# Kernel tuning notes

Hardware: AMD Instinct MI355X
Metric: run time of the kernel (lower is better)

## Reference

```python
import jax, jax.numpy as jnp
import numpy as np

D_MODEL = 1024
D_COND = 512
N_HEADS = 16
D_HEAD = D_MODEL // N_HEADS
DIM_FF = 4 * D_MODEL
EPS = 1e-5


def setup_inputs() -> dict:
    key = jax.random.key(0)
    ks = jax.random.split(key, 12)
    B, S = 2, 2048
    s = 0.02
    return {
        "x": jax.random.normal(ks[0], (B, S, D_MODEL), jnp.float32),
        "cond": jax.random.normal(ks[1], (B, S, D_COND), jnp.float32),
        # AdaLN1 proj (stored as (in, out) so y = h @ W + b)
        "p1_w": jax.random.normal(ks[2], (D_COND, 2 * D_MODEL), jnp.float32) * s,
        "p1_b": jax.random.normal(ks[3], (2 * D_MODEL,), jnp.float32) * s,
        "qkv_w": jax.random.normal(ks[4], (D_MODEL, 3 * D_MODEL), jnp.float32) * s,
        "attn_out_w": jax.random.normal(ks[5], (D_MODEL, D_MODEL), jnp.float32) * s,
        "p2_w": jax.random.normal(ks[6], (D_COND, 2 * D_MODEL), jnp.float32) * s,
        "p2_b": jax.random.normal(ks[7], (2 * D_MODEL,), jnp.float32) * s,
        "ffn_w1": jax.random.normal(ks[8], (D_MODEL, DIM_FF), jnp.float32) * s,
        "ffn_b1": jax.random.normal(ks[9], (DIM_FF,), jnp.float32) * s,
        "ffn_w2": jax.random.normal(ks[10], (DIM_FF, D_MODEL), jnp.float32) * s,
        "ffn_b2": jax.random.normal(ks[11], (D_MODEL,), jnp.float32) * s,
    }


def _adaln(x, cond, w, b):
    # LayerNorm without affine, then (1+gamma)*xn + beta with gamma,beta from cond
    gb = jax.nn.silu(cond) @ w + b            # (B,S,2D)
    gamma, beta = jnp.split(gb, 2, axis=-1)
    mu = jnp.mean(x, axis=-1, keepdims=True)
    var = jnp.mean((x - mu) ** 2, axis=-1, keepdims=True)
    xn = (x - mu) * jax.lax.rsqrt(var + EPS)
    return xn * (1.0 + gamma) + beta


def reference(x, cond, p1_w, p1_b, qkv_w, attn_out_w, p2_w, p2_b,
              ffn_w1, ffn_b1, ffn_w2, ffn_b2):
    B, S, D = x.shape
    H, d = N_HEADS, D_HEAD
    scale = d ** -0.5

    residual = x
    h = _adaln(x, cond, p1_w, p1_b)
    qkv = h @ qkv_w                            # (B,S,3D)
    q, k, v = jnp.split(qkv, 3, axis=-1)
    q = q.reshape(B, S, H, d).transpose(0, 2, 1, 3)   # (B,H,S,d)
    k = k.reshape(B, S, H, d).transpose(0, 2, 1, 3)
    v = v.reshape(B, S, H, d).transpose(0, 2, 1, 3)

    scores = jnp.einsum("bhqd,bhkd->bhqk", q, k) * scale
    attn = jax.nn.softmax(scores, axis=-1)
    out = jnp.einsum("bhqk,bhkd->bhqd", attn, v)      # (B,H,S,d)
    out = out.transpose(0, 2, 1, 3).reshape(B, S, D)
    x = residual + out @ attn_out_w

    residual = x
    h = _adaln(x, cond, p2_w, p2_b)
    ff = jax.nn.gelu(h @ ffn_w1 + ffn_b1, approximate=False) @ ffn_w2 + ffn_b2
    return residual + ff
```

## Files before the change

kernel.cpp:

```cpp
#include <hip/hip_runtime.h>
#include <math.h>

#define D_MODEL 1024
#define SEQ 2048
#define NTOK 4096

typedef __attribute__((ext_vector_type(8))) short bf16x8;
typedef __attribute__((ext_vector_type(4))) float f32x4;

__device__ __forceinline__ unsigned short f2bf(float f) {
    union { float f; unsigned u; } v; v.f = f;
    unsigned r = v.u + 0x7FFFu + ((v.u >> 16) & 1u);
    return (unsigned short)(r >> 16);
}
__device__ __forceinline__ float bf2f(unsigned short u) {
    union { unsigned u; float f; } v; v.u = ((unsigned)u) << 16; return v.f;
}
__device__ __forceinline__ unsigned pk2bf(float x, float y) {
    union { float f; unsigned u; } a, b;
    a.f = x; b.f = y;
    return ((b.u + 0x8000u) & 0xFFFF0000u) | ((a.u + 0x8000u) >> 16);
}

__device__ __forceinline__ void ld_g2l(const void* g, void* l) {
    __builtin_amdgcn_global_load_lds(
        (const __attribute__((address_space(1))) void*)g,
        (__attribute__((address_space(3))) void*)l, 16, 0, 0);
}

__global__ __launch_bounds__(256) void prep_weights(
    const float* __restrict__ p1, const float* __restrict__ p2,
    const float* __restrict__ qkvw, const float* __restrict__ attnw,
    const float* __restrict__ f1, const float* __restrict__ f2,
    const float* __restrict__ cond,
    unsigned short* __restrict__ wt_cond, unsigned short* __restrict__ wt_qkv,
    unsigned short* __restrict__ wt_attn, unsigned short* __restrict__ wt_ffn1,
    unsigned short* __restrict__ wt_ffn2, unsigned short* __restrict__ siluc)
{
    const int t = blockIdx.x;
    if (t >= 3584) {
        const int base = (t - 3584) * 1024 + threadIdx.x;
#pragma unroll
        for (int i = 0; i < 4; i++) {
            const int idx = base + i * 256;
            float4 v = ((const float4*)cond)[idx];
            ushort4 o;
            o.x = f2bf(v.x / (1.f + expf(-v.x)));
            o.y = f2bf(v.y / (1.f + expf(-v.y)));
            o.z = f2bf(v.z / (1.f + expf(-v.z)));
            o.w = f2bf(v.w / (1.f + expf(-v.w)));
            ((ushort4*)siluc)[idx] = o;
        }
        return;
    }
    const float* src; unsigned short* dst; int K, N, lt;
    if (t < 512)       { src = (t < 256) ? p1 : p2;
                         dst = wt_cond + (t < 256 ? 0 : 2048 * 512);
                         K = 512;  N = 2048; lt = t & 255; }
    else if (t < 1280) { src = qkvw;  dst = wt_qkv;  K = 1024; N = 3072; lt = t - 512; }
    else if (t < 1536) { src = attnw; dst = wt_attn; K = 1024; N = 1024; lt = t - 1280; }
    else if (t < 2560) { src = f1;    dst = wt_ffn1; K = 1024; N = 4096; lt = t - 1536; }
    else               { src = f2;    dst = wt_ffn2; K = 4096; N = 1024; lt = t - 2560; }
    const int ntile = N >> 6;
    const int n0 = (lt % ntile) * 64, k0 = (lt / ntile) * 64;

    __shared__ float tile[64][65];
    const int tx = threadIdx.x & 15, ty = threadIdx.x >> 4;
#pragma unroll
    for (int i = 0; i < 4; i++) {
        const int k = ty + i * 16;
        float4 v = *(const float4*)&src[(size_t)(k0 + k) * N + n0 + tx * 4];
        tile[k][tx * 4 + 0] = v.x; tile[k][tx * 4 + 1] = v.y;
        tile[k][tx * 4 + 2] = v.z; tile[k][tx * 4 + 3] = v.w;
    }
    __syncthreads();
#pragma unroll
    for (int i = 0; i < 4; i++) {
        const int n = ty + i * 16;
        ushort4 o;
        o.x = f2bf(tile[tx * 4 + 0][n]); o.y = f2bf(tile[tx * 4 + 1][n]);
        o.z = f2bf(tile[tx * 4 + 2][n]); o.w = f2bf(tile[tx * 4 + 3][n]);
        *(ushort4*)&dst[(size_t)(n0 + n) * K + k0 + tx * 4] = o;
    }
}

#define EPI_GB   0
#define EPI_QKV  1
#define EPI_PROJ 2
#define EPI_FFN1 3
#define EPI_FFN2 4

template<int EPI, int BM>
__global__ __launch_bounds__(256) void gemm_bf16(
    const unsigned short* __restrict__ A,
    const unsigned short* __restrict__ Bt,
    const float* __restrict__ bias, const float* __restrict__ bias2,
    const float* __restrict__ res,
    void* __restrict__ Cv,
    unsigned short* __restrict__ qb, unsigned short* __restrict__ kb,
    unsigned short* __restrict__ vtb,
    int K)
{
    constexpr int WM = BM / 2;
    constexpr int MT = WM / 16;
    __shared__ __align__(16) unsigned short As[BM * 64];
    __shared__ __align__(16) unsigned short Bs[128 * 64];
    const int tid = threadIdx.x;
    const int lane = tid & 63, w = tid >> 6;
    const int cc = lane & 15, quad = lane >> 4;
    const int wm = (w >> 1) * WM, wn = (w & 1) * 64;
    const int m0 = blockIdx.y * BM, n0 = blockIdx.x * 128;

    f32x4 acc[MT][4];
#pragma unroll
    for (int i = 0; i < MT; i++)
#pragma unroll
        for (int j = 0; j < 4; j++) acc[i][j] = (f32x4)0.f;

    for (int k0 = 0; k0 < K; k0 += 64) {
        __syncthreads();
#pragma unroll
        for (int i = 0; i < BM / 32; i++) {
            const int idx = i * 256 + tid;
            const int row = idx >> 3, c = idx & 7;
            const int kc = (c ^ (row & 7)) << 3;
            ld_g2l(&A[(size_t)(m0 + row) * K + k0 + kc], &As[idx << 3]);
        }
#pragma unroll
        for (int i = 0; i < 4; i++) {
            const int idx = i * 256 + tid;
            const int row = idx >> 3, c = idx & 7;
            const int kc = (c ^ (row & 7)) << 3;
            ld_g2l(&Bt[(size_t)(n0 + row) * K + k0 + kc], &Bs[idx << 3]);
        }
        __syncthreads();
#pragma unroll
        for (int ks = 0; ks < 2; ks++) {
            bf16x8 af[MT], bfr[4];
            const int pc = (((ks << 2) | quad) ^ (cc & 7)) << 3;
#pragma unroll
            for (int t = 0; t < MT; t++)
                af[t]  = *(const bf16x8*)&As[(wm + t * 16 + cc) * 64 + pc];
#pragma unroll
            for (int t = 0; t < 4; t++)
                bfr[t] = *(const bf16x8*)&Bs[(wn + t * 16 + cc) * 64 + pc];
#pragma unroll
            for (int mt = 0; mt < MT; mt++)
#pragma unroll
                for (int nt = 0; nt < 4; nt++)
                    acc[mt][nt] = __builtin_amdgcn_mfma_f32_16x16x32_bf16(
                        af[mt], bfr[nt], acc[mt][nt], 0, 0, 0);
        }
    }

    if (EPI == EPI_GB) {
        unsigned short* C = (unsigned short*)Cv;
#pragma unroll
        for (int mt = 0; mt < MT; mt++)
#pragma unroll
        for (int r = 0; r < 4; r++) {
            const int m = m0 + wm + mt * 16 + quad * 4 + r;
#pragma unroll
            for (int nt = 0; nt < 4; nt++) {
                const int n = n0 + wn + nt * 16 + cc;
                const float b = (n < 2048) ? bias[n] : bias2[n - 2048];
                C[(size_t)m * 4096 + n] = f2bf(acc[mt][nt][r] + b);
            }
        }
    } else if (EPI == EPI_PROJ) {
        float* C = (float*)Cv;
#pragma unroll
        for (int mt = 0; mt < MT; mt++)
#pragma unroll
        for (int r = 0; r < 4; r++) {
            const int m = m0 + wm + mt * 16 + quad * 4 + r;
#pragma unroll
            for (int nt = 0; nt < 4; nt++) {
                const int n = n0 + wn + nt * 16 + cc;
                C[(size_t)m * 1024 + n] = acc[mt][nt][r] + res[(size_t)m * 1024 + n];
            }
        }
    } else if (EPI == EPI_FFN1) {
        unsigned short* C = (unsigned short*)Cv;
#pragma unroll
        for (int mt = 0; mt < MT; mt++)
#pragma unroll
        for (int r = 0; r < 4; r++) {
            const int m = m0 + wm + mt * 16 + quad * 4 + r;
#pragma unroll
            for (int nt = 0; nt < 4; nt++) {
                const int n = n0 + wn + nt * 16 + cc;
                float v = acc[mt][nt][r] + bias[n];
                v = 0.5f * v * (1.f + erff(v * 0.70710678118654752f));
                C[(size_t)m * 4096 + n] = f2bf(v);
            }
        }
    } else if (EPI == EPI_FFN2) {
        float* C = (float*)Cv;
#pragma unroll
        for (int mt = 0; mt < MT; mt++)
#pragma unroll
        for (int r = 0; r < 4; r++) {
            const int m = m0 + wm + mt * 16 + quad * 4 + r;
#pragma unroll
            for (int nt = 0; nt < 4; nt++) {
                const int n = n0 + wn + nt * 16 + cc;
                C[(size_t)m * 1024 + n] = acc[mt][nt][r] + bias[n] + res[(size_t)m * 1024 + n];
            }
        }
    } else {
        const int region = n0 >> 10;
        const int b = m0 >> 11;
        if (region < 2) {
            unsigned short* dst = region ? kb : qb;
            const float sc = region ? 1.0f : 0.125f * 1.44269504088896340736f;
#pragma unroll
            for (int mt = 0; mt < MT; mt++)
#pragma unroll
            for (int r = 0; r < 4; r++) {
                const int m = m0 + wm + mt * 16 + quad * 4 + r;
                const int s = m & 2047;
#pragma unroll
                for (int nt = 0; nt < 4; nt++) {
                    const int n = (n0 + wn + nt * 16 + cc) & 1023;
                    const int hh = n >> 6, d = n & 63;
                    dst[(((size_t)b * 16 + hh) * 2048 + s) * 64 + d] =
                        f2bf(acc[mt][nt][r] * sc);
                }
            }
        } else {
            const int sb = (m0 + wm) & 2047;
#pragma unroll
            for (int mt = 0; mt < MT; mt++) {
                const int kpos = sb + ((mt >> 1) << 5) + (quad << 3) + ((mt & 1) << 2);
#pragma unroll
                for (int nt = 0; nt < 4; nt++) {
                    const int n = (n0 + wn + nt * 16 + cc) & 1023;
                    const int hh = n >> 6, d = n & 63;
                    ushort4 o;
                    o.x = f2bf(acc[mt][nt][0]); o.y = f2bf(acc[mt][nt][1]);
                    o.z = f2bf(acc[mt][nt][2]); o.w = f2bf(acc[mt][nt][3]);
                    *(ushort4*)&vtb[(((size_t)b * 16 + hh) * 64 + d) * 2048 + kpos] = o;
                }
            }
        }
    }
}

__global__ __launch_bounds__(256) void attn_mfma(
    const unsigned short* __restrict__ qb, const unsigned short* __restrict__ kb,
    const unsigned short* __restrict__ vtb, unsigned short* __restrict__ out)
{
    __shared__ __align__(16) unsigned short ks[64 * 64];
    __shared__ __align__(16) unsigned short vts[64 * 64];

    const int tid = threadIdx.x;
    const int lane = tid & 63, w = tid >> 6;
    const int c = lane & 15, quad = lane >> 4;
    const int bh = blockIdx.y;
    const int q0 = blockIdx.x * 128;

    bf16x8 qf[2][2];
#pragma unroll
    for (int qs = 0; qs < 2; qs++) {
        const size_t base = (((size_t)bh * 2048) + q0 + w * 32 + qs * 16 + c) * 64 + quad * 8;
        qf[qs][0] = *(const bf16x8*)&qb[base];
        qf[qs][1] = *(const bf16x8*)&qb[base + 32];
    }

    f32x4 of[2][4];
#pragma unroll
    for (int qs = 0; qs < 2; qs++)
#pragma unroll
        for (int i = 0; i < 4; i++) of[qs][i] = (f32x4)0.f;
    float l[2] = {0.f, 0.f};

    const size_t kbase = ((size_t)bh * 2048) * 64;
    const size_t vbase = ((size_t)bh * 64) * 2048;

    for (int kk = 0; kk < SEQ; kk += 64) {
        __syncthreads();
#pragma unroll
        for (int i = 0; i < 2; i++) {
            const int idx = i * 256 + tid;
            const int row = idx >> 3, pc = idx & 7;
            const int lc = pc ^ (row & 7);
            ld_g2l(&kb[kbase + (size_t)(kk + row) * 64 + lc * 8], &ks[idx << 3]);
        }
#pragma unroll
        for (int i = 0; i < 2; i++) {
            const int idx = i * 256 + tid;
            const int row = idx >> 3, pc = idx & 7;
            const int lc = pc ^ (row & 7);
            ld_g2l(&vtb[vbase + (size_t)row * 2048 + kk + lc * 8], &vts[idx << 3]);
        }
        __syncthreads();

        f32x4 sc[2][4];
#pragma unroll
        for (int qs = 0; qs < 2; qs++)
#pragma unroll
            for (int t = 0; t < 4; t++) sc[qs][t] = (f32x4)0.f;
#pragma unroll
        for (int t = 0; t < 4; t++) {
#pragma unroll
            for (int kh = 0; kh < 2; kh++) {
                const int phys = ((kh * 4 + quad) ^ (c & 7)) << 3;
                bf16x8 kf = *(const bf16x8*)&ks[(t * 16 + c) * 64 + phys];
#pragma unroll
                for (int qs = 0; qs < 2; qs++)
                    sc[qs][t] = __builtin_amdgcn_mfma_f32_16x16x32_bf16(
                        kf, qf[qs][kh], sc[qs][t], 0, 0, 0);
            }
        }

        bf16x8 pb[2][2];
#pragma unroll
        for (int qs = 0; qs < 2; qs++) {
#pragma unroll
            for (int t = 0; t < 4; t++)
#pragma unroll
                for (int r = 0; r < 4; r++) {
                    const float p = exp2f(sc[qs][t][r]);
                    sc[qs][t][r] = p;
                    l[qs] += p;
                }
#pragma unroll
            for (int kh = 0; kh < 2; kh++) {
                union { int4 i; bf16x8 v; } u;
                u.i.x = pk2bf(sc[qs][2 * kh][0],     sc[qs][2 * kh][1]);
                u.i.y = pk2bf(sc[qs][2 * kh][2],     sc[qs][2 * kh][3]);
                u.i.z = pk2bf(sc[qs][2 * kh + 1][0], sc[qs][2 * kh + 1][1]);
                u.i.w = pk2bf(sc[qs][2 * kh + 1][2], sc[qs][2 * kh + 1][3]);
                pb[qs][kh] = u.v;
            }
        }

#pragma unroll
        for (int dt = 0; dt < 4; dt++) {
#pragma unroll
            for (int kh = 0; kh < 2; kh++) {
                const int phys = ((kh * 4 + quad) ^ (c & 7)) << 3;
                bf16x8 vf = *(const bf16x8*)&vts[(dt * 16 + c) * 64 + phys];
#pragma unroll
                for (int qs = 0; qs < 2; qs++)
                    of[qs][dt] = __builtin_amdgcn_mfma_f32_16x16x32_bf16(
                        vf, pb[qs][kh], of[qs][dt], 0, 0, 0);
            }
        }
    }

    const int b = bh >> 4, hh = bh & 15;
#pragma unroll
    for (int qs = 0; qs < 2; qs++) {
        float lq = l[qs];
        lq += __shfl_xor(lq, 16, 64);
        lq += __shfl_xor(lq, 32, 64);
        const float inv = 1.f / lq;
        const size_t row = (size_t)(b * 2048 + q0 + w * 32 + qs * 16 + c);
#pragma unroll
        for (int dt = 0; dt < 4; dt++) {
            ushort4 o;
            o.x = f2bf(of[qs][dt][0] * inv); o.y = f2bf(of[qs][dt][1] * inv);
            o.z = f2bf(of[qs][dt][2] * inv); o.w = f2bf(of[qs][dt][3] * inv);
            *(ushort4*)&out[row * 1024 + hh * 64 + dt * 16 + quad * 4] = o;
        }
    }
}

__global__ __launch_bounds__(256) void adaln_bf(
    const float* __restrict__ x, const unsigned short* __restrict__ gb, int gboff,
    unsigned short* __restrict__ h)
{
    const int row = blockIdx.x;
    const float* xr = x + (size_t)row * D_MODEL;
    float vals[4];
    float s = 0.f, ss = 0.f;
#pragma unroll
    for (int i = 0; i < 4; i++) {
        float v = xr[threadIdx.x + i * 256];
        vals[i] = v;
        s += v; ss += v * v;
    }
#pragma unroll
    for (int off = 1; off < 64; off <<= 1) {
        s  += __shfl_xor(s, off, 64);
        ss += __shfl_xor(ss, off, 64);
    }
    __shared__ float red[8];
    const int wave = threadIdx.x >> 6;
    if ((threadIdx.x & 63) == 0) { red[wave] = s; red[4 + wave] = ss; }
    __syncthreads();
    s  = red[0] + red[1] + red[2] + red[3];
    ss = red[4] + red[5] + red[6] + red[7];
    const float mu = s * (1.f / 1024.f);
    const float var = ss * (1.f / 1024.f) - mu * mu;
    const float rstd = rsqrtf(var + 1e-5f);
    const unsigned short* g  = gb + (size_t)row * 4096 + gboff;
    const unsigned short* be = g + 1024;
    unsigned short* hr = h + (size_t)row * 1024;
#pragma unroll
    for (int i = 0; i < 4; i++) {
        const int c = threadIdx.x + i * 256;
        hr[c] = f2bf((vals[i] - mu) * rstd * (1.f + bf2f(g[c])) + bf2f(be[c]));
    }
}

extern "C" void kernel_launch(void* const* d_in, const int* in_sizes, int n_in,
                              void* d_out, int out_size, void* d_ws, size_t ws_size,
                              hipStream_t stream)
{
    const float* x      = (const float*)d_in[0];
    const float* cond   = (const float*)d_in[1];
    const float* p1_w   = (const float*)d_in[2];
    const float* p1_b   = (const float*)d_in[3];
    const float* qkv_w  = (const float*)d_in[4];
    const float* attn_w = (const float*)d_in[5];
    const float* p2_w   = (const float*)d_in[6];
    const float* p2_b   = (const float*)d_in[7];
    const float* ffn_w1 = (const float*)d_in[8];
    const float* ffn_b1 = (const float*)d_in[9];
    const float* ffn_w2 = (const float*)d_in[10];
    const float* ffn_b2 = (const float*)d_in[11];
    float* out = (float*)d_out;

    char* ws = (char*)d_ws;
    const size_t MB = 1024ull * 1024ull;
    unsigned short* wt_cond = (unsigned short*)(ws);
    unsigned short* wt_qkv  = (unsigned short*)(ws + 4 * MB);
    unsigned short* wt_attn = (unsigned short*)(ws + 10 * MB);
    unsigned short* wt_ffn1 = (unsigned short*)(ws + 12 * MB);
    unsigned short* wt_ffn2 = (unsigned short*)(ws + 20 * MB);
    unsigned short* siluc   = (unsigned short*)(ws + 28 * MB);
    unsigned short* gb      = (unsigned short*)(ws + 32 * MB);
    unsigned short* h       = (unsigned short*)(ws + 64 * MB);
    float*          x1      = (float*)(ws + 72 * MB);
    unsigned short* qb      = (unsigned short*)(ws + 88 * MB);
    unsigned short* kb      = (unsigned short*)(ws + 96 * MB);
    unsigned short* vtb     = (unsigned short*)(ws + 104 * MB);
    unsigned short* attnb   = (unsigned short*)(ws + 112 * MB);
    unsigned short* ff1     = (unsigned short*)(ws + 88 * MB);

    dim3 blk(256);

    prep_weights<<<dim3(4096), blk, 0, stream>>>(
        p1_w, p2_w, qkv_w, attn_w, ffn_w1, ffn_w2, cond,
        wt_cond, wt_qkv, wt_attn, wt_ffn1, wt_ffn2, siluc);

    gemm_bf16<EPI_GB, 128><<<dim3(32, 32), blk, 0, stream>>>(
        siluc, wt_cond, p1_b, p2_b, nullptr, gb, nullptr, nullptr, nullptr, 512);
    adaln_bf<<<NTOK, blk, 0, stream>>>(x, gb, 0, h);
    gemm_bf16<EPI_QKV, 128><<<dim3(24, 32), blk, 0, stream>>>(
        h, wt_qkv, nullptr, nullptr, nullptr, nullptr, qb, kb, vtb, 1024);
    attn_mfma<<<dim3(SEQ / 128, 32), blk, 0, stream>>>(qb, kb, vtb, attnb);
    gemm_bf16<EPI_PROJ, 64><<<dim3(8, 64), blk, 0, stream>>>(
        attnb, wt_attn, nullptr, nullptr, x, x1, nullptr, nullptr, nullptr, 1024);
    adaln_bf<<<NTOK, blk, 0, stream>>>(x1, gb, 2048, h);
    gemm_bf16<EPI_FFN1, 128><<<dim3(32, 32), blk, 0, stream>>>(
        h, wt_ffn1, ffn_b1, nullptr, nullptr, ff1, nullptr, nullptr, nullptr, 1024);
    gemm_bf16<EPI_FFN2, 64><<<dim3(8, 64), blk, 0, stream>>>(
        ff1, wt_ffn2, ffn_b2, nullptr, x1, out, nullptr, nullptr, nullptr, 4096);
}
```

Measured before the change: 433.7 us.

## Split attention over two KV halves with merge kernel; vectorize AdaLN

The attention kernel now uses 512-thread blocks covering 256 queries and splits the key/value sequence into two halves along a new grid dimension. Each half writes unnormalized bf16 partial outputs and per-row softmax denominators into workspace buffers that are no longer live at that point. A new merge kernel adds the two partials and divides by the summed denominator. The goal is twice as many waves in flight, each doing a shorter KV loop, at the cost of an extra launch, partial-output traffic and an additional bf16 rounding step. AdaLN is also rewritten to use float4 and ushort4 loads and stores instead of scalar accesses.

```diff
diff --git a/kernel.cpp b/kernel.cpp
--- a/kernel.cpp
+++ b/kernel.cpp
@@ -247,9 +247,11 @@
     }
 }
 
-__global__ __launch_bounds__(256) void attn_mfma(
+__global__ __launch_bounds__(512) void attn_mfma(
     const unsigned short* __restrict__ qb, const unsigned short* __restrict__ kb,
-    const unsigned short* __restrict__ vtb, unsigned short* __restrict__ out)
+    const unsigned short* __restrict__ vtb,
+    unsigned short* __restrict__ Op0, unsigned short* __restrict__ Op1,
+    float* __restrict__ lp)
 {
     __shared__ __align__(16) unsigned short ks[64 * 64];
     __shared__ __align__(16) unsigned short vts[64 * 64];
@@ -258,7 +260,9 @@
     const int lane = tid & 63, w = tid >> 6;
     const int c = lane & 15, quad = lane >> 4;
     const int bh = blockIdx.y;
-    const int q0 = blockIdx.x * 128;
+    const int q0 = blockIdx.x * 256;
+    const int z = blockIdx.z;
+    const int kk0 = z * 1024;
 
     bf16x8 qf[2][2];
 #pragma unroll
@@ -278,22 +282,13 @@
     const size_t kbase = ((size_t)bh * 2048) * 64;
     const size_t vbase = ((size_t)bh * 64) * 2048;
 
-    for (int kk = 0; kk < SEQ; kk += 64) {
+    const int srow = tid >> 3, spc = tid & 7;
+    const int slc = spc ^ (srow & 7);
+
+    for (int kk = kk0; kk < kk0 + 1024; kk += 64) {
         __syncthreads();
-#pragma unroll
-        for (int i = 0; i < 2; i++) {
-            const int idx = i * 256 + tid;
-            const int row = idx >> 3, pc = idx & 7;
-            const int lc = pc ^ (row & 7);
-            ld_g2l(&kb[kbase + (size_t)(kk + row) * 64 + lc * 8], &ks[idx << 3]);
-        }
-#pragma unroll
-        for (int i = 0; i < 2; i++) {
-            const int idx = i * 256 + tid;
-            const int row = idx >> 3, pc = idx & 7;
-            const int lc = pc ^ (row & 7);
-            ld_g2l(&vtb[vbase + (size_t)row * 2048 + kk + lc * 8], &vts[idx << 3]);
-        }
+        ld_g2l(&kb[kbase + (size_t)(kk + srow) * 64 + slc * 8], &ks[tid << 3]);
+        ld_g2l(&vtb[vbase + (size_t)srow * 2048 + kk + slc * 8], &vts[tid << 3]);
         __syncthreads();
 
         f32x4 sc[2][4];
@@ -350,22 +345,47 @@
         }
     }
 
+    unsigned short* Op = z ? Op1 : Op0;
     const int b = bh >> 4, hh = bh & 15;
 #pragma unroll
     for (int qs = 0; qs < 2; qs++) {
         float lq = l[qs];
         lq += __shfl_xor(lq, 16, 64);
         lq += __shfl_xor(lq, 32, 64);
-        const float inv = 1.f / lq;
-        const size_t row = (size_t)(b * 2048 + q0 + w * 32 + qs * 16 + c);
+        const int q = q0 + w * 32 + qs * 16 + c;
+        if (lane < 16)
+            lp[((size_t)z * 32 + bh) * 2048 + q] = lq;
+        const size_t row = (size_t)(b * 2048 + q);
 #pragma unroll
         for (int dt = 0; dt < 4; dt++) {
             ushort4 o;
-            o.x = f2bf(of[qs][dt][0] * inv); o.y = f2bf(of[qs][dt][1] * inv);
-            o.z = f2bf(of[qs][dt][2] * inv); o.w = f2bf(of[qs][dt][3] * inv);
-            *(ushort4*)&out[row * 1024 + hh * 64 + dt * 16 + quad * 4] = o;
-        }
-    }
+            o.x = f2bf(of[qs][dt][0]); o.y = f2bf(of[qs][dt][1]);
+            o.z = f2bf(of[qs][dt][2]); o.w = f2bf(of[qs][dt][3]);
+            *(ushort4*)&Op[row * 1024 + hh * 64 + dt * 16 + quad * 4] = o;
+        }
+    }
+}
+
+__global__ __launch_bounds__(256) void merge_attn(
+    const unsigned short* __restrict__ Op0, const unsigned short* __restrict__ Op1,
+    const float* __restrict__ lp, unsigned short* __restrict__ attnb)
+{
+    const int row = blockIdx.x;
+    const int b = row >> 11, s = row & 2047;
+    const int tid = threadIdx.x;
+    const int n = tid * 4, h = tid >> 4;
+    const float l0 = lp[((size_t)b * 16 + h) * 2048 + s];
+    const float l1 = lp[((size_t)32 + b * 16 + h) * 2048 + s];
+    const float inv = 1.f / (l0 + l1);
+    const size_t off = (size_t)row * 1024 + n;
+    ushort4 a = *(const ushort4*)&Op0[off];
+    ushort4 bb = *(const ushort4*)&Op1[off];
+    ushort4 o;
+    o.x = f2bf((bf2f(a.x) + bf2f(bb.x)) * inv);
+    o.y = f2bf((bf2f(a.y) + bf2f(bb.y)) * inv);
+    o.z = f2bf((bf2f(a.z) + bf2f(bb.z)) * inv);
+    o.w = f2bf((bf2f(a.w) + bf2f(bb.w)) * inv);
+    *(ushort4*)&attnb[off] = o;
 }
 
 __global__ __launch_bounds__(256) void adaln_bf(
@@ -374,14 +394,9 @@
 {
     const int row = blockIdx.x;
     const float* xr = x + (size_t)row * D_MODEL;
-    float vals[4];
-    float s = 0.f, ss = 0.f;
-#pragma unroll
-    for (int i = 0; i < 4; i++) {
-        float v = xr[threadIdx.x + i * 256];
-        vals[i] = v;
-        s += v; ss += v * v;
-    }
+    float4 v = ((const float4*)xr)[threadIdx.x];
+    float s = v.x + v.y + v.z + v.w;
+    float ss = v.x * v.x + v.y * v.y + v.z * v.z + v.w * v.w;
 #pragma unroll
     for (int off = 1; off < 64; off <<= 1) {
         s  += __shfl_xor(s, off, 64);
@@ -396,14 +411,15 @@
     const float mu = s * (1.f / 1024.f);
     const float var = ss * (1.f / 1024.f) - mu * mu;
     const float rstd = rsqrtf(var + 1e-5f);
-    const unsigned short* g  = gb + (size_t)row * 4096 + gboff;
-    const unsigned short* be = g + 1024;
-    unsigned short* hr = h + (size_t)row * 1024;
-#pragma unroll
-    for (int i = 0; i < 4; i++) {
-        const int c = threadIdx.x + i * 256;
-        hr[c] = f2bf((vals[i] - mu) * rstd * (1.f + bf2f(g[c])) + bf2f(be[c]));
-    }
+    const int c = threadIdx.x * 4;
+    ushort4 g4 = *(const ushort4*)&gb[(size_t)row * 4096 + gboff + c];
+    ushort4 b4 = *(const ushort4*)&gb[(size_t)row * 4096 + gboff + 1024 + c];
+    ushort4 o;
+    o.x = f2bf((v.x - mu) * rstd * (1.f + bf2f(g4.x)) + bf2f(b4.x));
+    o.y = f2bf((v.y - mu) * rstd * (1.f + bf2f(g4.y)) + bf2f(b4.y));
+    o.z = f2bf((v.z - mu) * rstd * (1.f + bf2f(g4.z)) + bf2f(b4.z));
+    o.w = f2bf((v.w - mu) * rstd * (1.f + bf2f(g4.w)) + bf2f(b4.w));
+    *(ushort4*)&h[(size_t)row * 1024 + c] = o;
 }
 
 extern "C" void kernel_launch(void* const* d_in, const int* in_sizes, int n_in,
@@ -440,6 +456,9 @@
     unsigned short* vtb     = (unsigned short*)(ws + 104 * MB);
     unsigned short* attnb   = (unsigned short*)(ws + 112 * MB);
     unsigned short* ff1     = (unsigned short*)(ws + 88 * MB);
+    unsigned short* Op0     = (unsigned short*)(ws);
+    unsigned short* Op1     = (unsigned short*)(ws + 64 * MB);
+    float*          lp      = (float*)(ws + 28 * MB);
 
     dim3 blk(256);
 
@@ -452,7 +471,9 @@
     adaln_bf<<<NTOK, blk, 0, stream>>>(x, gb, 0, h);
     gemm_bf16<EPI_QKV, 128><<<dim3(24, 32), blk, 0, stream>>>(
         h, wt_qkv, nullptr, nullptr, nullptr, nullptr, qb, kb, vtb, 1024);
-    attn_mfma<<<dim3(SEQ / 128, 32), blk, 0, stream>>>(qb, kb, vtb, attnb);
+    attn_mfma<<<dim3(SEQ / 256, 32, 2), dim3(512), 0, stream>>>(
+        qb, kb, vtb, Op0, Op1, lp);
+    merge_attn<<<dim3(NTOK), blk, 0, stream>>>(Op0, Op1, lp, attnb);
     gemm_bf16<EPI_PROJ, 64><<<dim3(8, 64), blk, 0, stream>>>(
         attnb, wt_attn, nullptr, nullptr, x, x1, nullptr, nullptr, nullptr, 1024);
     adaln_bf<<<NTOK, blk, 0, stream>>>(x1, gb, 2048, h);
```

Result: faster. 418.6 us (-3.5%).
